# Kernel optimization log

Measured on AMD Instinct MI355X. Metric: run time of the kernel, lower is better.

## Reference

```python
import jax, jax.numpy as jnp
import numpy as np

B, C, H, W = 16, 256, 64, 64
K = 1024


def setup_inputs() -> dict:
    key = jax.random.key(0)
    k1, k2 = jax.random.split(key)
    z = jax.random.normal(k1, (B, C, H, W), dtype=jnp.float32)
    codebook = jax.random.normal(k2, (K, C), dtype=jnp.float32)
    return {"z": z, "codebook": codebook}


def reference(z, codebook):
    # assign: nearest-code indices via squared euclidean distance
    b, c, h, w = z.shape
    zf = jnp.transpose(z, (0, 2, 3, 1)).reshape(-1, c)            # [N, C]
    # ||z||^2 - 2 z.cb^T + ||cb||^2  -> [N, K]
    dists = (jnp.sum(zf * zf, axis=1, keepdims=True)
             - 2.0 * jnp.einsum('nc,kc->nk', zf, codebook)
             + jnp.sum(codebook * codebook, axis=1)[None, :])
    idx = jnp.argmin(dists, axis=1)                                # [N]
    indices = idx.reshape(b, 1, h, w)                              # [B,1,H,W]
    # embed_code: gather codebook rows, back to BCHW
    zq = codebook[idx].reshape(b, h, w, c)                         # [B,H,W,C]
    zq = jnp.transpose(zq, (0, 3, 1, 2))                           # [B,C,H,W]
    return zq, indices
```

## Files before the change

kernel.cpp:

```cpp
#include <hip/hip_runtime.h>


#define HWSZ 4096
#define CDIM 256
#define KCODES 1024
#define NPIX 65536
#define ZQ_ELEMS (16 * 256 * 4096)
#define MARGIN 0.75f

#define WS_CBSWZ 0
#define WS_CBN64 524288
#define WS_CBN32 532480
#define WS_CNT   536576
#define WS_LISTS 536592

typedef __attribute__((ext_vector_type(8))) short bf16x8;
typedef __attribute__((ext_vector_type(4))) float f32x4;
typedef __attribute__((ext_vector_type(4))) unsigned short us4;

#define MFMA16(a, b, c) __builtin_amdgcn_mfma_f32_16x16x32_bf16(a, b, c, 0, 0, 0)

__device__ __forceinline__ unsigned short f2bf(float f) {
  unsigned u = __float_as_uint(f);
  unsigned r = u + 0x7FFFu + ((u >> 16) & 1u);
  return (unsigned short)(r >> 16);
}

__device__ __forceinline__ void gload_lds16(const void* g, void* l) {
  __builtin_amdgcn_global_load_lds(
      (const __attribute__((address_space(1))) unsigned int*)g,
      (__attribute__((address_space(3))) unsigned int*)l, 16, 0, 0);
}

__device__ __forceinline__ void ins3(unsigned& k1, unsigned& k2, unsigned& k3,
                                     unsigned k) {
  unsigned nk2, nk3;
  asm("v_med3_u32 %0, %1, %2, %3" : "=v"(nk2) : "v"(k1), "v"(k2), "v"(k));
  asm("v_med3_u32 %0, %1, %2, %3" : "=v"(nk3) : "v"(k2), "v"(k3), "v"(k));
  k1 = k1 < k ? k1 : k;
  k2 = nk2;
  k3 = nk3;
}

__device__ __forceinline__ float keyf(unsigned k) {
  return __uint_as_float(k & 0xFFFFFC00u);
}

__global__ void vq_prep(const float* __restrict__ cb,
                        unsigned short* __restrict__ cbswz,
                        double* __restrict__ cbn64,
                        float* __restrict__ cbn32p,
                        int* __restrict__ cnt) {
  const int t = threadIdx.x;
  if (blockIdx.x == 0 && t == 0) { cnt[0] = 0; cnt[1] = 0; }
  const int code = blockIdx.x * 4 + (t >> 6);
  const int lane = t & 63;
  const int c4 = lane * 4;

  float4 v = *(const float4*)(cb + (size_t)code * CDIM + c4);
  us4 hv;
  hv.x = f2bf(-2.f * v.x); hv.y = f2bf(-2.f * v.y);
  hv.z = f2bf(-2.f * v.z); hv.w = f2bf(-2.f * v.w);
  unsigned r = (unsigned)(code & 31);
  unsigned off = ((r << 9) + (unsigned)(c4 << 1)) ^ ((r & 7) << 4);
  *(us4*)((char*)cbswz + (size_t)(code >> 5) * 16384 + off) = hv;

  double s = (double)v.x * v.x;
  s = fma((double)v.y, (double)v.y, s);
  s = fma((double)v.z, (double)v.z, s);
  s = fma((double)v.w, (double)v.w, s);
#pragma unroll
  for (int o = 32; o; o >>= 1) s += __shfl_xor(s, o, 64);
  if (lane == 0) {
    cbn64[code] = s;
    cbn32p[code] = (float)s + 512.0f;
  }
}

__launch_bounds__(256)
__global__ void vq_stage1(const float* __restrict__ z,
                          const float* __restrict__ cb,
                          const unsigned short* __restrict__ cbswz,
                          const float* __restrict__ cbn32p,
                          float* __restrict__ out_zq,
                          float* __restrict__ out_idx,
                          int* __restrict__ cnt,
                          int* __restrict__ listA, int capA,
                          int* __restrict__ listB, int capB,
                          float* __restrict__ zws, int zcap) {
  extern __shared__ char smem[];
  const int t = threadIdx.x;
  const int w = t >> 6;
  const int lane = t & 63;
  const int lg = lane >> 4;
  const int lcode = lane & 15;
  const int p0 = blockIdx.x * 64;
  const int b = p0 >> 12;
  const int hw0 = p0 & (HWSZ - 1);
  const float* zb = z + (size_t)b * (CDIM * HWSZ) + hw0;

  {
    const char* gsrc = (const char*)cbswz + t * 16;
    char* ldst = smem + (w * 1024 + (lane >> 2) * 64) + (lane & 3) * 16;
#pragma unroll
    for (int j = 0; j < 4; ++j)
      gload_lds16(gsrc + j * 4096, ldst + j * 4096);
  }

  bf16x8 af[8];
  {
    const float* zr = zb + (w * 16 + lcode);
#pragma unroll
    for (int kk = 0; kk < 8; ++kk) {
      const int ch0 = kk * 32 + lg * 8;
      bf16x8 f;
#pragma unroll
      for (int j = 0; j < 8; ++j)
        f[j] = (short)f2bf(zr[(size_t)(ch0 + j) * HWSZ]);
      af[kk] = f;
    }
  }
  __syncthreads();

  unsigned k1[4], k2[4], k3[4];
#pragma unroll
  for (int q = 0; q < 4; ++q) {
    k1[q] = 0xFFFFFFFFu; k2[q] = 0xFFFFFFFFu; k3[q] = 0xFFFFFFFFu;
  }

  const unsigned rsw = ((unsigned)(lane & 7)) << 4;
  const unsigned kl16 = ((unsigned)lg) << 4;

  for (int c = 0; c < 32; ++c) {
    const char* rbuf = smem + (c & 1) * 16384;
    if (c < 31) {
      const char* gsrc = (const char*)cbswz + (c + 1) * 16384 + t * 16;
      char* ldst = smem + ((c + 1) & 1) * 16384 +
                   (w * 1024 + (lane >> 2) * 64) + (lane & 3) * 16;
#pragma unroll
      for (int j = 0; j < 4; ++j)
        gload_lds16(gsrc + j * 4096, ldst + j * 4096);
    }
#pragma unroll
    for (int cs = 0; cs < 2; ++cs) {
      const int r = cs * 16 + lcode;
      const unsigned base = ((unsigned)r << 9) + kl16;
      f32x4 acc = {0.f, 0.f, 0.f, 0.f};
#pragma unroll
      for (int kk = 0; kk < 8; ++kk) {
        bf16x8 bf = *(const bf16x8*)(rbuf + ((base + ((unsigned)kk << 6)) ^ rsw));
        acc = MFMA16(af[kk], bf, acc);
      }
      const unsigned code = (unsigned)(c * 32 + cs * 16 + lcode);
      const float cn = cbn32p[code];
#pragma unroll
      for (int q = 0; q < 4; ++q) {
        float m = cn + acc[q];
        unsigned key = (__float_as_uint(m) & 0xFFFFFC00u) | code;
        ins3(k1[q], k2[q], k3[q], key);
      }
    }
    __syncthreads();
  }

#pragma unroll
  for (int mask = 1; mask <= 8; mask <<= 1) {
#pragma unroll
    for (int q = 0; q < 4; ++q) {
      unsigned o1 = __shfl_xor(k1[q], mask, 64);
      unsigned o2 = __shfl_xor(k2[q], mask, 64);
      unsigned o3 = __shfl_xor(k3[q], mask, 64);
      ins3(k1[q], k2[q], k3[q], o1);
      ins3(k1[q], k2[q], k3[q], o2);
      ins3(k1[q], k2[q], k3[q], o3);
    }
  }

  int* sbest = (int*)smem;
  int* lcnt = (int*)(smem + 256);
  int* flp = (int*)(smem + 512);
  int* flq = (int*)(smem + 768);
  if (t == 0) *lcnt = 0;
  __syncthreads();

  if (lcode == 0) {
#pragma unroll
    for (int q = 0; q < 4; ++q) {
      int row = w * 16 + lg * 4 + q;
      int p = p0 + row;
      int i1 = (int)(k1[q] & 1023u);
      sbest[row] = i1;
      out_idx[p] = (float)i1;
      float f1 = keyf(k1[q]);
      float g2 = keyf(k2[q]) - f1;
      float g3 = keyf(k3[q]) - f1;
      if (g3 < MARGIN) {
        int pos = atomicAdd(cnt + 1, 1);
        if (pos < capB) listB[pos] = p;
      } else if (g2 < MARGIN) {
        int pos = atomicAdd(cnt, 1);
        if (pos < capA) {
          listA[2 * pos] = p | (i1 << 16);
          listA[2 * pos + 1] = (int)(k2[q] & 1023u) |
                               ((int)(k3[q] & 1023u) << 16);
          if (pos < zcap) {
            int li = atomicAdd(lcnt, 1);
            flp[li] = p;
            flq[li] = pos;
          }
        }
      }
    }
  }
  __syncthreads();

  {
    const int px = t & 63;
    const int best = sbest[px];
    const int ch0g = (t >> 6) * 64;
    const float* crow = cb + (size_t)best * CDIM + ch0g;
    float* ob = out_zq + (size_t)b * (CDIM * HWSZ) + (size_t)ch0g * HWSZ + hw0 + px;
#pragma unroll 4
    for (int c2 = 0; c2 < 64; c2 += 4) {
      float4 v = *(const float4*)(crow + c2);
      ob[(size_t)(c2 + 0) * HWSZ] = v.x;
      ob[(size_t)(c2 + 1) * HWSZ] = v.y;
      ob[(size_t)(c2 + 2) * HWSZ] = v.z;
      ob[(size_t)(c2 + 3) * HWSZ] = v.w;
    }
  }

  {
    const int nf = *lcnt;
    for (int e = 0; e < nf; ++e) {
      const int p = flp[e];
      const int slot = flq[e];
      const int bb = p >> 12;
      const int hh = p & (HWSZ - 1);
      zws[(size_t)slot * 256 + t] =
          z[(size_t)bb * (CDIM * HWSZ) + (size_t)t * HWSZ + hh];
    }
  }
}

__launch_bounds__(256)
__global__ void vq_resolve3(const float* __restrict__ z,
                            const float* __restrict__ cb,
                            const double* __restrict__ cbn64,
                            float* __restrict__ out_zq,
                            float* __restrict__ out_idx,
                            const int* __restrict__ cnt,
                            const int* __restrict__ listA, int capA,
                            const float* __restrict__ zws, int zcap) {
  const int lane = threadIdx.x & 63;
  const int wid = (blockIdx.x * blockDim.x + threadIdx.x) >> 6;
  const int nw = (gridDim.x * blockDim.x) >> 6;
  int n = cnt[0];
  if (n > capA) n = capA;

  for (int i = wid; i < n; i += nw) {
    const int e0 = listA[2 * i];
    const int e1 = listA[2 * i + 1];
    const int p = e0 & 0xFFFF;
    int cand[3];
    cand[0] = (e0 >> 16) & 1023;
    cand[1] = e1 & 0xFFFF;
    cand[2] = (e1 >> 16) & 1023;
    const int b = p >> 12;
    const int hw = p & (HWSZ - 1);
    const int ch0 = lane * 4;

    double zv[4];
    if (i < zcap) {
      float4 zf = ((const float4*)(zws + (size_t)i * 256))[lane];
      zv[0] = (double)zf.x; zv[1] = (double)zf.y;
      zv[2] = (double)zf.z; zv[3] = (double)zf.w;
    } else {
      const float* zb = z + (size_t)b * (CDIM * HWSZ) + hw;
#pragma unroll
      for (int j = 0; j < 4; ++j) zv[j] = (double)zb[(size_t)(ch0 + j) * HWSZ];
    }

    double d[3];
#pragma unroll
    for (int tt = 0; tt < 3; ++tt) {
      float4 cv = *(const float4*)(cb + (size_t)cand[tt] * CDIM + ch0);
      double s = zv[0] * (double)cv.x;
      s = fma(zv[1], (double)cv.y, s);
      s = fma(zv[2], (double)cv.z, s);
      s = fma(zv[3], (double)cv.w, s);
#pragma unroll
      for (int off = 32; off; off >>= 1) s += __shfl_xor(s, off, 64);
      d[tt] = fma(-2.0, s, cbn64[cand[tt]]);
    }

    double bd = d[0];
    int bi = cand[0];
#pragma unroll
    for (int tt = 1; tt < 3; ++tt) {
      bool takes = (d[tt] < bd) || (d[tt] == bd && cand[tt] < bi);
      bd = takes ? d[tt] : bd;
      bi = takes ? cand[tt] : bi;
    }

    if (lane == 0) out_idx[p] = (float)bi;
    float4 cv = *(const float4*)(cb + (size_t)bi * CDIM + ch0);
    float* ob = out_zq + (size_t)b * (CDIM * HWSZ) + hw;
    ob[(size_t)(ch0 + 0) * HWSZ] = cv.x;
    ob[(size_t)(ch0 + 1) * HWSZ] = cv.y;
    ob[(size_t)(ch0 + 2) * HWSZ] = cv.z;
    ob[(size_t)(ch0 + 3) * HWSZ] = cv.w;
  }
}

__launch_bounds__(256)
__global__ void vq_fullscan(const float* __restrict__ z,
                            const float* __restrict__ cb,
                            const double* __restrict__ cbn64,
                            float* __restrict__ out_zq,
                            float* __restrict__ out_idx,
                            const int* __restrict__ cnt,
                            const int* __restrict__ listB, int capB) {
  __shared__ double zl[256];
  __shared__ double sd[4];
  __shared__ int si[4];
  __shared__ int sfin;
  int n = cnt[1];
  if (n > capB) n = capB;
  const int t = threadIdx.x;
  const int w = t >> 6;
  const int lane = t & 63;

  for (int i = blockIdx.x; i < n; i += gridDim.x) {
    const int p = listB[i];
    const int b = p >> 12;
    const int hw = p & (HWSZ - 1);
    const float* zb = z + (size_t)b * (CDIM * HWSZ) + hw;
    zl[t] = (double)zb[(size_t)t * HWSZ];
    __syncthreads();

    const int g = t >> 2;
    const int sub = t & 3;
    const double* zq4 = zl + sub * 64;
    double bd = 1e300;
    int bi = 0;

    for (int j = 0; j < 16; ++j) {
      const int code = g + 64 * j;
      const float* crow = cb + (size_t)code * CDIM + sub * 64;
      double s = 0.0;
#pragma unroll
      for (int q4 = 0; q4 < 64; q4 += 4) {
        float4 cv = *(const float4*)(crow + q4);
        s = fma(zq4[q4 + 0], (double)cv.x, s);
        s = fma(zq4[q4 + 1], (double)cv.y, s);
        s = fma(zq4[q4 + 2], (double)cv.z, s);
        s = fma(zq4[q4 + 3], (double)cv.w, s);
      }
      s += __shfl_xor(s, 1, 64);
      s += __shfl_xor(s, 2, 64);
      double d = fma(-2.0, s, cbn64[code]);
      bool takes = (d < bd) || (d == bd && code < bi);
      bd = takes ? d : bd;
      bi = takes ? code : bi;
    }

#pragma unroll
    for (int off = 4; off <= 32; off <<= 1) {
      double od = __shfl_xor(bd, off, 64);
      int oi = __shfl_xor(bi, off, 64);
      bool takes = (od < bd) || (od == bd && oi < bi);
      bd = takes ? od : bd;
      bi = takes ? oi : bi;
    }
    if (lane == 0) { sd[w] = bd; si[w] = bi; }
    __syncthreads();
    if (t == 0) {
      double fd = sd[0];
      int fi = si[0];
#pragma unroll
      for (int k = 1; k < 4; ++k) {
        bool takes = (sd[k] < fd) || (sd[k] == fd && si[k] < fi);
        fd = takes ? sd[k] : fd;
        fi = takes ? si[k] : fi;
      }
      sfin = fi;
      out_idx[p] = (float)fi;
    }
    __syncthreads();
    const int best = sfin;
    float* ob = out_zq + (size_t)b * (CDIM * HWSZ) + hw;
    ob[(size_t)t * HWSZ] = cb[(size_t)best * CDIM + t];
    __syncthreads();
  }
}

extern "C" void kernel_launch(void* const* d_in, const int* in_sizes, int n_in,
                              void* d_out, int out_size, void* d_ws, size_t ws_size,
                              hipStream_t stream) {
  const float* z = (const float*)d_in[0];
  const float* cb = (const float*)d_in[1];
  float* out = (float*)d_out;
  float* out_zq = out;
  float* out_idx = out + ZQ_ELEMS;

  char* ws = (char*)d_ws;
  unsigned short* cbswz = (unsigned short*)(ws + WS_CBSWZ);
  double* cbn64 = (double*)(ws + WS_CBN64);
  float* cbn32p = (float*)(ws + WS_CBN32);
  int* cnt = (int*)(ws + WS_CNT);

  long long avail = (long long)ws_size - WS_LISTS;
  if (avail < 0) avail = 0;
  long long capA_ll = (avail / 4) / 8;
  if (capA_ll > NPIX) capA_ll = NPIX;
  int capA = (int)capA_ll;
  int* listA = (int*)(ws + WS_LISTS);
  long long rem = avail - (long long)capA * 8;
  long long capB_ll = rem / 8;
  if (capB_ll > NPIX) capB_ll = NPIX;
  if (capB_ll < 0) capB_ll = 0;
  int capB = (int)capB_ll;
  int* listB = (int*)(ws + WS_LISTS + (size_t)capA * 8);
  long long zoff = (WS_LISTS + (long long)capA * 8 + (long long)capB * 4 + 15) &
                   ~15LL;
  long long zcap_ll = ((long long)ws_size - zoff) / 1024;
  if (zcap_ll < 0) zcap_ll = 0;
  if (zcap_ll > capA) zcap_ll = capA;
  int zcap = (int)zcap_ll;
  float* zws = (float*)(ws + zoff);

  vq_prep<<<256, 256, 0, stream>>>(cb, cbswz, cbn64, cbn32p, cnt);
  vq_stage1<<<1024, 256, 32768, stream>>>(z, cb, cbswz, cbn32p, out_zq, out_idx,
                                          cnt, listA, capA, listB, capB,
                                          zws, zcap);
  vq_resolve3<<<1024, 256, 0, stream>>>(z, cb, cbn64, out_zq, out_idx,
                                        cnt, listA, capA, zws, zcap);
  vq_fullscan<<<256, 256, 0, stream>>>(z, cb, cbn64, out_zq, out_idx,
                                       cnt, listB, capB);
}
```

Before: 187.2 us.

## Split codebook across wave pairs so each B fragment feeds two pixel tiles

Stage 1 now gives each wave 32 pixels (two 16-pixel A tiles) and half of the codebook, so every LDS codebook fragment load feeds two MFMAs instead of one. The codebook layout is re-swizzled into 16-code halves to match. Codebook norms are staged once in LDS. The two halves' top-3 lists are merged through shared memory. The resolve and fullscan kernels also skip rewriting zq and indices when the refined winner equals the stage-1 choice. This trades more A-fragment registers and an extra merge step for half the LDS reads per MFMA and fewer redundant global writes.

```diff
diff --git a/kernel.cpp b/kernel.cpp
--- a/kernel.cpp
+++ b/kernel.cpp
@@ -61,9 +61,10 @@
   us4 hv;
   hv.x = f2bf(-2.f * v.x); hv.y = f2bf(-2.f * v.y);
   hv.z = f2bf(-2.f * v.z); hv.w = f2bf(-2.f * v.w);
-  unsigned r = (unsigned)(code & 31);
+  const int K = (code >> 9) * 32 + ((code >> 4) & 31);
+  unsigned r = (unsigned)(code & 15);
   unsigned off = ((r << 9) + (unsigned)(c4 << 1)) ^ ((r & 7) << 4);
-  *(us4*)((char*)cbswz + (size_t)(code >> 5) * 16384 + off) = hv;
+  *(us4*)((char*)cbswz + (size_t)K * 8192 + off) = hv;
 
   double s = (double)v.x * v.x;
   s = fma((double)v.y, (double)v.y, s);
@@ -94,22 +95,32 @@
   const int lane = t & 63;
   const int lg = lane >> 4;
   const int lcode = lane & 15;
+  const int h = w >> 1;
+  const int q = w & 1;
   const int p0 = blockIdx.x * 64;
   const int b = p0 >> 12;
   const int hw0 = p0 & (HWSZ - 1);
   const float* zb = z + (size_t)b * (CDIM * HWSZ) + hw0;
 
+  float* nrm = (float*)(smem + 32768);
   {
-    const char* gsrc = (const char*)cbswz + t * 16;
-    char* ldst = smem + (w * 1024 + (lane >> 2) * 64) + (lane & 3) * 16;
+    float4 nv = *(const float4*)(cbn32p + t * 4);
+    *(float4*)(nrm + t * 4) = nv;
+  }
+
+  {
+    const char* gsrc = (const char*)cbswz + (size_t)(q * 32) * 8192 +
+                       (h * 4) * 1024 + lane * 16;
+    char* ldst = smem + q * 8192 + (h * 4) * 1024 + lane * 16;
 #pragma unroll
     for (int j = 0; j < 4; ++j)
-      gload_lds16(gsrc + j * 4096, ldst + j * 4096);
-  }
-
-  bf16x8 af[8];
-  {
-    const float* zr = zb + (w * 16 + lcode);
+      gload_lds16(gsrc + j * 1024, ldst + j * 1024);
+  }
+
+  bf16x8 af[2][8];
+#pragma unroll
+  for (int T = 0; T < 2; ++T) {
+    const float* zr = zb + (h * 32 + T * 16 + lcode);
 #pragma unroll
     for (int kk = 0; kk < 8; ++kk) {
       const int ch0 = kk * 32 + lg * 8;
@@ -117,97 +128,113 @@
 #pragma unroll
       for (int j = 0; j < 8; ++j)
         f[j] = (short)f2bf(zr[(size_t)(ch0 + j) * HWSZ]);
-      af[kk] = f;
+      af[T][kk] = f;
     }
   }
   __syncthreads();
 
-  unsigned k1[4], k2[4], k3[4];
-#pragma unroll
-  for (int q = 0; q < 4; ++q) {
-    k1[q] = 0xFFFFFFFFu; k2[q] = 0xFFFFFFFFu; k3[q] = 0xFFFFFFFFu;
-  }
-
-  const unsigned rsw = ((unsigned)(lane & 7)) << 4;
-  const unsigned kl16 = ((unsigned)lg) << 4;
+  unsigned k1[2][4], k2[2][4], k3[2][4];
+#pragma unroll
+  for (int T = 0; T < 2; ++T)
+#pragma unroll
+    for (int q4 = 0; q4 < 4; ++q4) {
+      k1[T][q4] = 0xFFFFFFFFu; k2[T][q4] = 0xFFFFFFFFu; k3[T][q4] = 0xFFFFFFFFu;
+    }
+
+  const unsigned rsw = ((unsigned)(lcode & 7)) << 4;
+  const unsigned rbase = ((unsigned)lcode << 9) + (((unsigned)lg) << 4);
+  const char* myhalf = smem + q * 8192;
+  const int nrm0 = q * 512 + lcode;
 
   for (int c = 0; c < 32; ++c) {
-    const char* rbuf = smem + (c & 1) * 16384;
+    const char* rbuf = myhalf + (c & 1) * 16384;
     if (c < 31) {
-      const char* gsrc = (const char*)cbswz + (c + 1) * 16384 + t * 16;
-      char* ldst = smem + ((c + 1) & 1) * 16384 +
-                   (w * 1024 + (lane >> 2) * 64) + (lane & 3) * 16;
+      const char* gsrc = (const char*)cbswz + (size_t)(q * 32 + c + 1) * 8192 +
+                         (h * 4) * 1024 + lane * 16;
+      char* ldst = smem + ((c + 1) & 1) * 16384 + q * 8192 +
+                   (h * 4) * 1024 + lane * 16;
 #pragma unroll
       for (int j = 0; j < 4; ++j)
-        gload_lds16(gsrc + j * 4096, ldst + j * 4096);
-    }
-#pragma unroll
-    for (int cs = 0; cs < 2; ++cs) {
-      const int r = cs * 16 + lcode;
-      const unsigned base = ((unsigned)r << 9) + kl16;
-      f32x4 acc = {0.f, 0.f, 0.f, 0.f};
-#pragma unroll
-      for (int kk = 0; kk < 8; ++kk) {
-        bf16x8 bf = *(const bf16x8*)(rbuf + ((base + ((unsigned)kk << 6)) ^ rsw));
-        acc = MFMA16(af[kk], bf, acc);
-      }
-      const unsigned code = (unsigned)(c * 32 + cs * 16 + lcode);
-      const float cn = cbn32p[code];
-#pragma unroll
-      for (int q = 0; q < 4; ++q) {
-        float m = cn + acc[q];
+        gload_lds16(gsrc + j * 1024, ldst + j * 1024);
+    }
+    f32x4 acc0 = {0.f, 0.f, 0.f, 0.f};
+    f32x4 acc1 = {0.f, 0.f, 0.f, 0.f};
+#pragma unroll
+    for (int kk = 0; kk < 8; ++kk) {
+      bf16x8 bf = *(const bf16x8*)(rbuf + ((rbase + ((unsigned)kk << 6)) ^ rsw));
+      acc0 = MFMA16(af[0][kk], bf, acc0);
+      acc1 = MFMA16(af[1][kk], bf, acc1);
+    }
+    const unsigned code = (unsigned)(nrm0 + c * 16);
+    const float cn = nrm[code];
+#pragma unroll
+    for (int T = 0; T < 2; ++T)
+#pragma unroll
+      for (int q4 = 0; q4 < 4; ++q4) {
+        float m = cn + ((T == 0) ? acc0[q4] : acc1[q4]);
         unsigned key = (__float_as_uint(m) & 0xFFFFFC00u) | code;
-        ins3(k1[q], k2[q], k3[q], key);
-      }
-    }
+        ins3(k1[T][q4], k2[T][q4], k3[T][q4], key);
+      }
     __syncthreads();
   }
 
 #pragma unroll
   for (int mask = 1; mask <= 8; mask <<= 1) {
 #pragma unroll
-    for (int q = 0; q < 4; ++q) {
-      unsigned o1 = __shfl_xor(k1[q], mask, 64);
-      unsigned o2 = __shfl_xor(k2[q], mask, 64);
-      unsigned o3 = __shfl_xor(k3[q], mask, 64);
-      ins3(k1[q], k2[q], k3[q], o1);
-      ins3(k1[q], k2[q], k3[q], o2);
-      ins3(k1[q], k2[q], k3[q], o3);
-    }
-  }
-
-  int* sbest = (int*)smem;
-  int* lcnt = (int*)(smem + 256);
-  int* flp = (int*)(smem + 512);
-  int* flq = (int*)(smem + 768);
+    for (int T = 0; T < 2; ++T)
+#pragma unroll
+      for (int q4 = 0; q4 < 4; ++q4) {
+        unsigned o1 = __shfl_xor(k1[T][q4], mask, 64);
+        unsigned o2 = __shfl_xor(k2[T][q4], mask, 64);
+        unsigned o3 = __shfl_xor(k3[T][q4], mask, 64);
+        ins3(k1[T][q4], k2[T][q4], k3[T][q4], o1);
+        ins3(k1[T][q4], k2[T][q4], k3[T][q4], o2);
+        ins3(k1[T][q4], k2[T][q4], k3[T][q4], o3);
+      }
+  }
+
+  unsigned* mk = (unsigned*)smem;
+  int* lcnt = (int*)(smem + 2304);
   if (t == 0) *lcnt = 0;
+  if (lcode == 0) {
+#pragma unroll
+    for (int T = 0; T < 2; ++T)
+#pragma unroll
+      for (int q4 = 0; q4 < 4; ++q4) {
+        int row = h * 32 + T * 16 + lg * 4 + q4;
+        unsigned* d = mk + (row * 2 + q) * 3;
+        d[0] = k1[T][q4]; d[1] = k2[T][q4]; d[2] = k3[T][q4];
+      }
+  }
   __syncthreads();
 
-  if (lcode == 0) {
-#pragma unroll
-    for (int q = 0; q < 4; ++q) {
-      int row = w * 16 + lg * 4 + q;
-      int p = p0 + row;
-      int i1 = (int)(k1[q] & 1023u);
-      sbest[row] = i1;
-      out_idx[p] = (float)i1;
-      float f1 = keyf(k1[q]);
-      float g2 = keyf(k2[q]) - f1;
-      float g3 = keyf(k3[q]) - f1;
-      if (g3 < MARGIN) {
-        int pos = atomicAdd(cnt + 1, 1);
-        if (pos < capB) listB[pos] = p;
-      } else if (g2 < MARGIN) {
-        int pos = atomicAdd(cnt, 1);
-        if (pos < capA) {
-          listA[2 * pos] = p | (i1 << 16);
-          listA[2 * pos + 1] = (int)(k2[q] & 1023u) |
-                               ((int)(k3[q] & 1023u) << 16);
-          if (pos < zcap) {
-            int li = atomicAdd(lcnt, 1);
-            flp[li] = p;
-            flq[li] = pos;
-          }
+  int* sbest = (int*)(smem + 2048);
+  int* flp = (int*)(smem + 2560);
+  int* flq = (int*)(smem + 2816);
+  if (t < 64) {
+    unsigned a1 = mk[t * 6 + 0], a2 = mk[t * 6 + 1], a3 = mk[t * 6 + 2];
+    ins3(a1, a2, a3, mk[t * 6 + 3]);
+    ins3(a1, a2, a3, mk[t * 6 + 4]);
+    ins3(a1, a2, a3, mk[t * 6 + 5]);
+    const int p = p0 + t;
+    const int i1 = (int)(a1 & 1023u);
+    sbest[t] = i1;
+    out_idx[p] = (float)i1;
+    float f1 = keyf(a1);
+    float g2 = keyf(a2) - f1;
+    float g3 = keyf(a3) - f1;
+    if (g3 < MARGIN) {
+      int pos = atomicAdd(cnt + 1, 1);
+      if (pos < capB) listB[pos] = p;
+    } else if (g2 < MARGIN) {
+      int pos = atomicAdd(cnt, 1);
+      if (pos < capA) {
+        listA[2 * pos] = p | (i1 << 16);
+        listA[2 * pos + 1] = (int)(a2 & 1023u) | ((int)(a3 & 1023u) << 16);
+        if (pos < zcap) {
+          int li = atomicAdd(lcnt, 1);
+          flp[li] = p;
+          flq[li] = pos;
         }
       }
     }
@@ -303,13 +330,15 @@
       bi = takes ? cand[tt] : bi;
     }
 
-    if (lane == 0) out_idx[p] = (float)bi;
-    float4 cv = *(const float4*)(cb + (size_t)bi * CDIM + ch0);
-    float* ob = out_zq + (size_t)b * (CDIM * HWSZ) + hw;
-    ob[(size_t)(ch0 + 0) * HWSZ] = cv.x;
-    ob[(size_t)(ch0 + 1) * HWSZ] = cv.y;
-    ob[(size_t)(ch0 + 2) * HWSZ] = cv.z;
-    ob[(size_t)(ch0 + 3) * HWSZ] = cv.w;
+    if (bi != cand[0]) {
+      if (lane == 0) out_idx[p] = (float)bi;
+      float4 cv = *(const float4*)(cb + (size_t)bi * CDIM + ch0);
+      float* ob = out_zq + (size_t)b * (CDIM * HWSZ) + hw;
+      ob[(size_t)(ch0 + 0) * HWSZ] = cv.x;
+      ob[(size_t)(ch0 + 1) * HWSZ] = cv.y;
+      ob[(size_t)(ch0 + 2) * HWSZ] = cv.z;
+      ob[(size_t)(ch0 + 3) * HWSZ] = cv.w;
+    }
   }
 }
 
@@ -384,13 +413,16 @@
         fd = takes ? sd[k] : fd;
         fi = takes ? si[k] : fi;
       }
-      sfin = fi;
-      out_idx[p] = (float)fi;
+      const int old = (int)out_idx[p];
+      if (fi != old) out_idx[p] = (float)fi;
+      sfin = (fi != old) ? fi : -1;
     }
     __syncthreads();
     const int best = sfin;
-    float* ob = out_zq + (size_t)b * (CDIM * HWSZ) + hw;
-    ob[(size_t)t * HWSZ] = cb[(size_t)best * CDIM + t];
+    if (best >= 0) {
+      float* ob = out_zq + (size_t)b * (CDIM * HWSZ) + hw;
+      ob[(size_t)t * HWSZ] = cb[(size_t)best * CDIM + t];
+    }
     __syncthreads();
   }
 }
@@ -431,7 +463,7 @@
   float* zws = (float*)(ws + zoff);
 
   vq_prep<<<256, 256, 0, stream>>>(cb, cbswz, cbn64, cbn32p, cnt);
-  vq_stage1<<<1024, 256, 32768, stream>>>(z, cb, cbswz, cbn32p, out_zq, out_idx,
+  vq_stage1<<<1024, 256, 36864, stream>>>(z, cb, cbswz, cbn32p, out_zq, out_idx,
                                           cnt, listA, capA, listB, capB,
                                           zws, zcap);
   vq_resolve3<<<1024, 256, 0, stream>>>(z, cb, cbn64, out_zq, out_idx,
```

Result: faster. 164.0 us (-12.4%).
